# Kernel optimization log

Hardware: AMD Instinct MI355X
Metric: run time of the kernel (lower is better)

The kernel has to match this reference:

```python
import jax, jax.numpy as jnp
import numpy as np

N = 50000       # nodes
E = 800000      # edges (before self-loops)
NFEAT = 256
NHID = 16       # per-head hidden dim
HEADS = 8
NCLASS = 16
NEG_SLOPE = 0.2  # PyG GATConv default leaky-relu slope


def setup_inputs() -> dict:
    key = jax.random.key(0)
    ks = jax.random.split(key, 10)
    s = 0.05  # weight scale for numerical sanity
    return {
        "x": jax.random.normal(ks[0], (N, NFEAT), jnp.float32),
        "edge_index": jax.random.randint(ks[1], (2, E), 0, N, dtype=jnp.int32),
        "W1": jax.random.normal(ks[2], (NFEAT, HEADS * NHID), jnp.float32) * s,
        "att_src1": jax.random.normal(ks[3], (HEADS, NHID), jnp.float32) * s,
        "att_dst1": jax.random.normal(ks[4], (HEADS, NHID), jnp.float32) * s,
        "b1": jnp.zeros((HEADS * NHID,), jnp.float32),
        "W2": jax.random.normal(ks[5], (HEADS * NHID, NCLASS), jnp.float32) * s,
        "att_src2": jax.random.normal(ks[6], (1, NCLASS), jnp.float32) * s,
        "att_dst2": jax.random.normal(ks[7], (1, NCLASS), jnp.float32) * s,
        "b2": jnp.zeros((NCLASS,), jnp.float32),
    }


def gat_conv(x, edge_index, W, a_src, a_dst, b, heads, out_c, concat):
    """Faithful PyG GATConv (eval mode: dropout off, add_self_loops=True)."""
    n = x.shape[0]
    loop = jnp.arange(n, dtype=edge_index.dtype)
    src = jnp.concatenate([edge_index[0], loop])  # [E+N]
    dst = jnp.concatenate([edge_index[1], loop])  # [E+N]
    h = (x @ W).reshape(n, heads, out_c)          # [N, H, C]
    # per-node attention logits
    alpha_src = jnp.einsum('nhc,hc->nh', h, a_src)  # [N, H]
    alpha_dst = jnp.einsum('nhc,hc->nh', h, a_dst)  # [N, H]
    e = jax.nn.leaky_relu(alpha_src[src] + alpha_dst[dst], NEG_SLOPE)  # [E+N, H]
    # segment softmax over incoming edges of each dst node (self-loop guarantees nonempty)
    m = jax.lax.stop_gradient(jax.ops.segment_max(e, dst, num_segments=n))
    p = jnp.exp(e - m[dst])
    denom = jax.ops.segment_sum(p, dst, num_segments=n)
    a = p / denom[dst]                              # [E+N, H]
    out = jax.ops.segment_sum(a[:, :, None] * h[src], dst, num_segments=n)  # [N, H, C]
    out = out.reshape(n, heads * out_c) if concat else out.mean(axis=1)
    return out + b


def reference(x, edge_index, W1, att_src1, att_dst1, b1, W2, att_src2, att_dst2, b2):
    h1 = jax.nn.elu(gat_conv(x, edge_index, W1, att_src1, att_dst1, b1, HEADS, NHID, True))
    return gat_conv(h1, edge_index, W2, att_src2, att_dst2, b2, 1, NCLASS, False)
```

## Files before the change

kernel.cpp:

```cpp
#include <hip/hip_runtime.h>
#include <hip/hip_bf16.h>

#define NNODES 50000
#define NEDGES 800000
#define NFEATS 256
#define NHID 16
#define HEADS 8
#define NCLS 16
#define NEG_SLOPE 0.2f
#define TOTE (NEDGES + NNODES)
#define RSTRIDE 64
#define NBUCK 196
#define NPB 256
#define BCAP 4864
#define S1_EPT 16

typedef __attribute__((ext_vector_type(8))) short short8;
typedef __attribute__((ext_vector_type(4))) float floatx4;

static __device__ __forceinline__ short f2bf(float f) {
    __hip_bfloat16 b = __float2bfloat16(f);
    return *reinterpret_cast<short*>(&b);
}

#define AS1 __attribute__((address_space(1)))
#define AS3 __attribute__((address_space(3)))

static __device__ __forceinline__ void ld_lds16(const void* g, void* l) {
#if __has_builtin(__builtin_amdgcn_global_load_lds)
    __builtin_amdgcn_global_load_lds((const AS1 void*)g, (AS3 void*)l, 16, 0, 0);
#endif
}


__global__ __launch_bounds__(256) void k_bin(const int* __restrict__ ei,
                                             int* __restrict__ gcnt, int2* __restrict__ barr) {
    __shared__ int lcnt[NBUCK], lbase[NBUCK];
    int tid = threadIdx.x;
    if (tid < NBUCK) lcnt[tid] = 0;
    __syncthreads();
    int e0 = blockIdx.x * (256 * S1_EPT) + tid;
    int s[S1_EPT], d[S1_EPT], rk[S1_EPT];
#pragma unroll
    for (int k = 0; k < S1_EPT; k++) {
        int e = e0 + k * 256;
        bool v = e < TOTE;
        int ss = 0, dd = 0;
        if (v) {
            if (e < NEDGES) { ss = ei[e]; dd = ei[NEDGES + e]; }
            else            { ss = e - NEDGES; dd = ss; }
        }
        s[k] = ss; d[k] = dd;
        rk[k] = v ? atomicAdd(&lcnt[dd >> 8], 1) : -1;
    }
    __syncthreads();
    if (tid < NBUCK) lbase[tid] = lcnt[tid] ? atomicAdd(&gcnt[tid], lcnt[tid]) : 0;
    __syncthreads();
#pragma unroll
    for (int k = 0; k < S1_EPT; k++) {
        if (rk[k] >= 0) {
            int b = d[k] >> 8;
            int pos = lbase[b] + rk[k];
            if (pos < BCAP) barr[(size_t)b * BCAP + pos] = make_int2(s[k], d[k]);
        }
    }
}


__global__ __launch_bounds__(256) void k_csr(const int* __restrict__ gcnt,
                                             const int2* __restrict__ barr,
                                             int* __restrict__ cnt, int* __restrict__ csr) {
    __shared__ int lcnt[NPB];
    __shared__ unsigned short lcsr[NPB * 65];
    int b = blockIdx.x, tid = threadIdx.x;
    lcnt[tid] = 0;
    __syncthreads();
    int n = min(gcnt[b], BCAP);
    int nodeBase = b << 8;
    for (int i = tid; i < n; i += 256) {
        int2 e = barr[(size_t)b * BCAP + i];
        int ln = e.y - nodeBase;
        int r = atomicAdd(&lcnt[ln], 1);
        if (r < RSTRIDE) lcsr[ln * 65 + r] = (unsigned short)e.x;
    }
    __syncthreads();
    int node = nodeBase + tid;
    if (node < NNODES) cnt[node] = min(lcnt[tid], RSTRIDE);
    for (int i = tid; i < NPB * RSTRIDE; i += 256) {
        int nn = nodeBase + (i >> 6);
        if (nn < NNODES)
            csr[(size_t)nodeBase * RSTRIDE + i] = (int)lcsr[(i >> 6) * 65 + (i & 63)];
    }
}


__global__ void k_prepw(const float* __restrict__ W, const float* __restrict__ a_s,
                        const float* __restrict__ a_d, short* __restrict__ Wsw) {
    int t = blockIdx.x * 256 + threadIdx.x;
    if (t >= 4608) return;
    short8 b;
    if (t < 4096) {
        int kc = t >> 9, nt = (t >> 6) & 7, lane = t & 63;
        int quad = lane >> 4, lo = lane & 15;
#pragma unroll
        for (int j = 0; j < 8; j++)
            b[j] = f2bf(W[(size_t)(kc * 32 + quad * 8 + j) * 128 + nt * 16 + lo]);
    } else {
        int t2 = t - 4096;
        int kc = t2 >> 6, lane = t2 & 63;
        int quad = lane >> 4, lo = lane & 15;
        int h = lo & 7;
        const float* av = (lo < 8) ? (a_s + h * 16) : (a_d + h * 16);
#pragma unroll
        for (int j = 0; j < 8; j++) {
            int k = kc * 32 + quad * 8 + j;
            float acc = 0.f;
#pragma unroll
            for (int c = 0; c < 16; c++) acc += W[(size_t)k * 128 + h * 16 + c] * av[c];
            b[j] = f2bf(acc);
        }
    }
    *(short8*)(Wsw + (size_t)t * 8) = b;
}


__global__ __launch_bounds__(256) void k_gemm1(const float* __restrict__ x,
                                               const short* __restrict__ Wsw,
                                               __hip_bfloat16* __restrict__ h1,
                                               float* __restrict__ as1, float* __restrict__ ad1) {
    __shared__ short bsw[32768];
    int tid  = threadIdx.x;
    int wave = tid >> 6;
    int lane = tid & 63;
    int quad = lane >> 4;
    int lo   = lane & 15;

#if __has_builtin(__builtin_amdgcn_global_load_lds)
    {
        const char* gsrc = (const char*)Wsw + (size_t)wave * 1024 + (size_t)lane * 16;
        char* ldst = (char*)bsw + wave * 1024;
#pragma unroll
        for (int it = 0; it < 16; it++)
            ld_lds16(gsrc + it * 4096, ldst + it * 4096);
    }
#else
    {
        const uint4* g4 = (const uint4*)Wsw;
        uint4* l4 = (uint4*)bsw;
#pragma unroll
        for (int it = 0; it < 16; it++) l4[it * 256 + tid] = g4[it * 256 + tid];
    }
#endif
    short8 wafr[8];
#pragma unroll
    for (int kc = 0; kc < 8; kc++)
        wafr[kc] = *(const short8*)(Wsw + (size_t)(4096 + kc * 64 + lane) * 8);
    __syncthreads();

    int rowBase = blockIdx.x * 128 + wave * 32;
    const float* xa[2];
#pragma unroll
    for (int mt = 0; mt < 2; mt++) {
        int row = rowBase + mt * 16 + lo;
        row = (row < NNODES) ? row : (NNODES - 1);
        xa[mt] = x + (size_t)row * 256 + quad * 8;
    }

    floatx4 acc[2][8], accA[2];
#pragma unroll
    for (int mt = 0; mt < 2; mt++) {
        accA[mt] = (floatx4){0.f, 0.f, 0.f, 0.f};
#pragma unroll
        for (int nt = 0; nt < 8; nt++) acc[mt][nt] = (floatx4){0.f, 0.f, 0.f, 0.f};
    }

    float4 a0[2], a1[2];
#pragma unroll
    for (int mt = 0; mt < 2; mt++) {
        a0[mt] = *(const float4*)(xa[mt]);
        a1[mt] = *(const float4*)(xa[mt] + 4);
    }

    for (int kc = 0; kc < 8; kc++) {
        float4 n0[2], n1[2];
        if (kc < 7) {
#pragma unroll
            for (int mt = 0; mt < 2; mt++) {
                n0[mt] = *(const float4*)(xa[mt] + (kc + 1) * 32);
                n1[mt] = *(const float4*)(xa[mt] + (kc + 1) * 32 + 4);
            }
        }
        short8 afr[2];
#pragma unroll
        for (int mt = 0; mt < 2; mt++) {
            union { short8 s; __hip_bfloat162 h[4]; } u;
            u.h[0] = __float22bfloat162_rn(make_float2(a0[mt].x, a0[mt].y));
            u.h[1] = __float22bfloat162_rn(make_float2(a0[mt].z, a0[mt].w));
            u.h[2] = __float22bfloat162_rn(make_float2(a1[mt].x, a1[mt].y));
            u.h[3] = __float22bfloat162_rn(make_float2(a1[mt].z, a1[mt].w));
            afr[mt] = u.s;
        }
#pragma unroll
        for (int nt = 0; nt < 8; nt++) {
            short8 bfr = *(const short8*)&bsw[((kc * 8 + nt) * 64 + lane) * 8];
            acc[0][nt] = __builtin_amdgcn_mfma_f32_16x16x32_bf16(afr[0], bfr, acc[0][nt], 0, 0, 0);
            acc[1][nt] = __builtin_amdgcn_mfma_f32_16x16x32_bf16(afr[1], bfr, acc[1][nt], 0, 0, 0);
        }
        accA[0] = __builtin_amdgcn_mfma_f32_16x16x32_bf16(afr[0], wafr[kc], accA[0], 0, 0, 0);
        accA[1] = __builtin_amdgcn_mfma_f32_16x16x32_bf16(afr[1], wafr[kc], accA[1], 0, 0, 0);
#pragma unroll
        for (int mt = 0; mt < 2; mt++) { a0[mt] = n0[mt]; a1[mt] = n1[mt]; }
    }

#pragma unroll
    for (int mt = 0; mt < 2; mt++)
#pragma unroll
        for (int nt = 0; nt < 8; nt++)
#pragma unroll
            for (int reg = 0; reg < 4; reg++) {
                int row = rowBase + mt * 16 + quad * 4 + reg;
                int col = nt * 16 + lo;
                if (row < NNODES)
                    h1[(size_t)row * 128 + col] = __float2bfloat16(acc[mt][nt][reg]);
            }
#pragma unroll
    for (int mt = 0; mt < 2; mt++)
#pragma unroll
        for (int reg = 0; reg < 4; reg++) {
            int row = rowBase + mt * 16 + quad * 4 + reg;
            if (row < NNODES) {
                float v = accA[mt][reg];
                if (lo < 8) as1[(size_t)row * 8 + lo] = v;
                else        ad1[(size_t)row * 8 + (lo - 8)] = v;
            }
        }
}


__global__ __launch_bounds__(256) void k_agg1(const int* __restrict__ cnt, const int* __restrict__ csr,
                                              const __hip_bfloat16* __restrict__ h1,
                                              const float* __restrict__ as1, const float* __restrict__ ad1,
                                              const float* __restrict__ b1, __hip_bfloat16* __restrict__ h1act) {
    int node = blockIdx.x * 4 + (threadIdx.x >> 6);
    int lane = threadIdx.x & 63;
    if (node >= NNODES) return;
    int rs = node * RSTRIDE;
    int deg = min(cnt[node], RSTRIDE);
    int slot = lane >> 4;
    int cl   = lane & 15;
    int head = cl >> 1;
    float adst = ad1[node * 8 + head];

    float acc[8] = {0.f, 0.f, 0.f, 0.f, 0.f, 0.f, 0.f, 0.f};
    float s = 0.f;
    for (int base = 0; base < deg; base += 8) {
        int i0 = base + slot, i1 = base + 4 + slot;
        float p0 = 0.f, p1 = 0.f;
        union { short8 v; __hip_bfloat162 h[4]; } u0, u1;
        u0.v = (short8){0, 0, 0, 0, 0, 0, 0, 0};
        u1.v = (short8){0, 0, 0, 0, 0, 0, 0, 0};
        if (i0 < deg) {
            int sa = csr[rs + i0];
            u0.v = *(const short8*)(h1 + (size_t)sa * 128 + cl * 8);
            float e0 = as1[sa * 8 + head] + adst;
            e0 = (e0 > 0.f) ? e0 : NEG_SLOPE * e0;
            p0 = __expf(e0);
        }
        if (i1 < deg) {
            int sb = csr[rs + i1];
            u1.v = *(const short8*)(h1 + (size_t)sb * 128 + cl * 8);
            float e1 = as1[sb * 8 + head] + adst;
            e1 = (e1 > 0.f) ? e1 : NEG_SLOPE * e1;
            p1 = __expf(e1);
        }
        s += p0 + p1;
#pragma unroll
        for (int q = 0; q < 4; q++) {
            float2 f0 = __bfloat1622float2(u0.h[q]);
            float2 f1 = __bfloat1622float2(u1.h[q]);
            acc[q * 2]     = fmaf(p0, f0.x, fmaf(p1, f1.x, acc[q * 2]));
            acc[q * 2 + 1] = fmaf(p0, f0.y, fmaf(p1, f1.y, acc[q * 2 + 1]));
        }
    }
#pragma unroll
    for (int q = 0; q < 8; q++) {
        acc[q] += __shfl_xor(acc[q], 16);
        acc[q] += __shfl_xor(acc[q], 32);
    }
    s += __shfl_xor(s, 16);
    s += __shfl_xor(s, 32);
    if (slot == 0) {
        float is = 1.f / s;
        union { short8 v; short us[8]; } pk;
#pragma unroll
        for (int q = 0; q < 8; q++) {
            float v = acc[q] * is + b1[cl * 8 + q];
            v = (v > 0.f) ? v : (__expf(v) - 1.f);
            pk.us[q] = f2bf(v);
        }
        *(short8*)(h1act + (size_t)node * 128 + cl * 8) = pk.v;
    }
}


__global__ __launch_bounds__(256) void k_gemm2(const __hip_bfloat16* __restrict__ h1act,
                                               const float* __restrict__ W2,
                                               const float* __restrict__ a_src,
                                               const float* __restrict__ a_dst,
                                               float* __restrict__ h2,
                                               float* __restrict__ as2, float* __restrict__ ad2) {
    __shared__ float w[128 * 16];
    __shared__ float hr[16][129];
    int tid = threadIdx.x;
    int row0 = blockIdx.x * 16;
    for (int i = tid; i < 2048; i += 256) w[i] = W2[i];
    {
        int r = tid >> 4, k8 = (tid & 15) * 8;
        int gr = row0 + r;
        union { short8 v; __hip_bfloat162 h[4]; } u;
        if (gr < NNODES) u.v = *(const short8*)(h1act + (size_t)gr * 128 + k8);
        else             u.v = (short8){0, 0, 0, 0, 0, 0, 0, 0};
#pragma unroll
        for (int q = 0; q < 4; q++) {
            float2 f = __bfloat1622float2(u.h[q]);
            hr[r][k8 + q * 2]     = f.x;
            hr[r][k8 + q * 2 + 1] = f.y;
        }
    }
    __syncthreads();
    int r = tid >> 4, c = tid & 15;
    float acc = 0.f;
#pragma unroll 8
    for (int k = 0; k < 128; k++) acc += hr[r][k] * w[k * 16 + c];
    int gr = row0 + r;
    if (gr < NNODES) h2[(size_t)gr * 16 + c] = acc;
    float sv = acc * a_src[c];
    float dv = acc * a_dst[c];
#pragma unroll
    for (int o = 1; o <= 8; o <<= 1) {
        sv += __shfl_xor(sv, o);
        dv += __shfl_xor(dv, o);
    }
    if (c == 0 && gr < NNODES) { as2[gr] = sv; ad2[gr] = dv; }
}


__global__ __launch_bounds__(256) void k_agg2(const int* __restrict__ cnt, const int* __restrict__ csr,
                                              const float* __restrict__ h2, const float* __restrict__ as2,
                                              const float* __restrict__ ad2, const float* __restrict__ b2,
                                              float* __restrict__ out) {
    int node = blockIdx.x * 4 + (threadIdx.x >> 6);
    int lane = threadIdx.x & 63;
    if (node >= NNODES) return;
    int rs = node * RSTRIDE;
    int deg = min(cnt[node], RSTRIDE);
    int slot = lane >> 2;
    int c4   = lane & 3;
    float adst = ad2[node];

    float4 acc = make_float4(0.f, 0.f, 0.f, 0.f);
    float s = 0.f;
    for (int base = 0; base < deg; base += 16) {
        int i0 = base + slot;
        float p0 = 0.f;
        float4 r0 = make_float4(0.f, 0.f, 0.f, 0.f);
        if (i0 < deg) {
            int sa = csr[rs + i0];
            r0 = *(const float4*)(h2 + (size_t)sa * 16 + c4 * 4);
            float e0 = as2[sa] + adst;
            e0 = (e0 > 0.f) ? e0 : NEG_SLOPE * e0;
            p0 = __expf(e0);
        }
        s += p0;
        acc.x = fmaf(p0, r0.x, acc.x);
        acc.y = fmaf(p0, r0.y, acc.y);
        acc.z = fmaf(p0, r0.z, acc.z);
        acc.w = fmaf(p0, r0.w, acc.w);
    }
#pragma unroll
    for (int o = 4; o <= 32; o <<= 1) {
        acc.x += __shfl_xor(acc.x, o);
        acc.y += __shfl_xor(acc.y, o);
        acc.z += __shfl_xor(acc.z, o);
        acc.w += __shfl_xor(acc.w, o);
        s += __shfl_xor(s, o);
    }
    if (slot == 0) {
        float is = 1.f / s;
        float4 o4;
        o4.x = acc.x * is + b2[c4 * 4 + 0];
        o4.y = acc.y * is + b2[c4 * 4 + 1];
        o4.z = acc.z * is + b2[c4 * 4 + 2];
        o4.w = acc.w * is + b2[c4 * 4 + 3];
        *(float4*)(out + (size_t)node * 16 + c4 * 4) = o4;
    }
}


extern "C" void kernel_launch(void* const* d_in, const int* in_sizes, int n_in,
                              void* d_out, int out_size, void* d_ws, size_t ws_size,
                              hipStream_t stream) {
    const float* x    = (const float*)d_in[0];
    const int*   ei   = (const int*)d_in[1];
    const float* W1   = (const float*)d_in[2];
    const float* a_s1 = (const float*)d_in[3];
    const float* a_d1 = (const float*)d_in[4];
    const float* b1   = (const float*)d_in[5];
    const float* W2   = (const float*)d_in[6];
    const float* a_s2 = (const float*)d_in[7];
    const float* a_d2 = (const float*)d_in[8];
    const float* b2   = (const float*)d_in[9];
    float* out = (float*)d_out;

    char* p = (char*)d_ws;
    auto alloc = [&](size_t bytes) -> char* {
        char* q = p;
        p += (bytes + 255) & ~(size_t)255;
        return q;
    };
    int*  gcnt = (int*)alloc(NBUCK * 4);
    int2* barr = (int2*)alloc((size_t)NBUCK * BCAP * 8);
    int*  cnt  = (int*)alloc((size_t)NNODES * 4);
    int*  csr  = (int*)alloc((size_t)NNODES * RSTRIDE * 4);
    short* Wsw = (short*)alloc((size_t)36864 * 2);
    __hip_bfloat16* h1 = (__hip_bfloat16*)alloc((size_t)NNODES * 128 * 2);
    float* as1 = (float*)alloc((size_t)NNODES * 8 * 4);
    float* ad1 = (float*)alloc((size_t)NNODES * 8 * 4);
    __hip_bfloat16* h1act = (__hip_bfloat16*)alloc((size_t)NNODES * 128 * 2);
    float* h2  = (float*)as1;
    float* as2 = (float*)barr;
    float* ad2 = (float*)(barr + NNODES);

    hipMemsetAsync(gcnt, 0, NBUCK * 4, stream);
    hipLaunchKernelGGL(k_bin,   dim3((TOTE + 4095) / 4096), dim3(256), 0, stream, ei, gcnt, barr);
    hipLaunchKernelGGL(k_csr,   dim3(NBUCK), dim3(256), 0, stream, gcnt, barr, cnt, csr);
    hipLaunchKernelGGL(k_prepw, dim3(18), dim3(256), 0, stream, W1, a_s1, a_d1, Wsw);
    hipLaunchKernelGGL(k_gemm1, dim3((NNODES + 127) / 128), dim3(256), 0, stream, x, Wsw, h1, as1, ad1);
    hipLaunchKernelGGL(k_agg1,  dim3((NNODES + 3) / 4), dim3(256), 0, stream, cnt, csr, h1, as1, ad1, b1, h1act);
    hipLaunchKernelGGL(k_gemm2, dim3((NNODES + 15) / 16), dim3(256), 0, stream, h1act, W2, a_s2, a_d2, h2, as2, ad2);
    hipLaunchKernelGGL(k_agg2,  dim3((NNODES + 3) / 4), dim3(256), 0, stream, cnt, csr, h2, as2, ad2, b2, out);
}
```

Measured before the change: 229.2 us.

## Pack binned edges into 32-bit words and preload CSR rows via wave shuffles

Edge bins now store a single 32-bit word (local dst in the high half, src in the low 16 bits) instead of an int2, halving bucket traffic. CSR writes skip slots beyond each node's degree. Both aggregation kernels load the whole 64-entry CSR row once per lane and broadcast neighbour indices with shuffles. They also process more edges per iteration (4 per slot in agg1, 2 in agg2) to expose more memory parallelism. Packing the source into 16 bits only works if node ids fit in 16 bits. With 50000 nodes they do, since the previous code already truncated sources to unsigned short, and the later reuse of barr for as2/ad2 still fits.

```diff
diff --git a/kernel.cpp b/kernel.cpp
--- a/kernel.cpp
+++ b/kernel.cpp
@@ -34,7 +34,7 @@
 
 
 __global__ __launch_bounds__(256) void k_bin(const int* __restrict__ ei,
-                                             int* __restrict__ gcnt, int2* __restrict__ barr) {
+                                             int* __restrict__ gcnt, int* __restrict__ barr) {
     __shared__ int lcnt[NBUCK], lbase[NBUCK];
     int tid = threadIdx.x;
     if (tid < NBUCK) lcnt[tid] = 0;
@@ -61,14 +61,15 @@
         if (rk[k] >= 0) {
             int b = d[k] >> 8;
             int pos = lbase[b] + rk[k];
-            if (pos < BCAP) barr[(size_t)b * BCAP + pos] = make_int2(s[k], d[k]);
+            if (pos < BCAP)
+                barr[(size_t)b * BCAP + pos] = ((d[k] & 255) << 16) | s[k];
         }
     }
 }
 
 
 __global__ __launch_bounds__(256) void k_csr(const int* __restrict__ gcnt,
-                                             const int2* __restrict__ barr,
+                                             const int* __restrict__ barr,
                                              int* __restrict__ cnt, int* __restrict__ csr) {
     __shared__ int lcnt[NPB];
     __shared__ unsigned short lcsr[NPB * 65];
@@ -78,18 +79,19 @@
     int n = min(gcnt[b], BCAP);
     int nodeBase = b << 8;
     for (int i = tid; i < n; i += 256) {
-        int2 e = barr[(size_t)b * BCAP + i];
-        int ln = e.y - nodeBase;
+        int e = barr[(size_t)b * BCAP + i];
+        int ln = e >> 16;
         int r = atomicAdd(&lcnt[ln], 1);
-        if (r < RSTRIDE) lcsr[ln * 65 + r] = (unsigned short)e.x;
+        if (r < RSTRIDE) lcsr[ln * 65 + r] = (unsigned short)(e & 0xFFFF);
     }
     __syncthreads();
     int node = nodeBase + tid;
     if (node < NNODES) cnt[node] = min(lcnt[tid], RSTRIDE);
     for (int i = tid; i < NPB * RSTRIDE; i += 256) {
-        int nn = nodeBase + (i >> 6);
-        if (nn < NNODES)
-            csr[(size_t)nodeBase * RSTRIDE + i] = (int)lcsr[(i >> 6) * 65 + (i & 63)];
+        int ln = i >> 6;
+        int nn = nodeBase + ln;
+        if (nn < NNODES && (i & 63) < min(lcnt[ln], RSTRIDE))
+            csr[(size_t)nodeBase * RSTRIDE + i] = (int)lcsr[ln * 65 + (i & 63)];
     }
 }
 
@@ -250,37 +252,36 @@
     int cl   = lane & 15;
     int head = cl >> 1;
     float adst = ad1[node * 8 + head];
+    int rowv = csr[rs + lane];
 
     float acc[8] = {0.f, 0.f, 0.f, 0.f, 0.f, 0.f, 0.f, 0.f};
     float s = 0.f;
-    for (int base = 0; base < deg; base += 8) {
-        int i0 = base + slot, i1 = base + 4 + slot;
-        float p0 = 0.f, p1 = 0.f;
-        union { short8 v; __hip_bfloat162 h[4]; } u0, u1;
-        u0.v = (short8){0, 0, 0, 0, 0, 0, 0, 0};
-        u1.v = (short8){0, 0, 0, 0, 0, 0, 0, 0};
-        if (i0 < deg) {
-            int sa = csr[rs + i0];
-            u0.v = *(const short8*)(h1 + (size_t)sa * 128 + cl * 8);
-            float e0 = as1[sa * 8 + head] + adst;
-            e0 = (e0 > 0.f) ? e0 : NEG_SLOPE * e0;
-            p0 = __expf(e0);
-        }
-        if (i1 < deg) {
-            int sb = csr[rs + i1];
-            u1.v = *(const short8*)(h1 + (size_t)sb * 128 + cl * 8);
-            float e1 = as1[sb * 8 + head] + adst;
-            e1 = (e1 > 0.f) ? e1 : NEG_SLOPE * e1;
-            p1 = __expf(e1);
-        }
-        s += p0 + p1;
-#pragma unroll
-        for (int q = 0; q < 4; q++) {
-            float2 f0 = __bfloat1622float2(u0.h[q]);
-            float2 f1 = __bfloat1622float2(u1.h[q]);
-            acc[q * 2]     = fmaf(p0, f0.x, fmaf(p1, f1.x, acc[q * 2]));
-            acc[q * 2 + 1] = fmaf(p0, f0.y, fmaf(p1, f1.y, acc[q * 2 + 1]));
-        }
+    for (int base = 0; base < deg; base += 16) {
+        int src[4]; float p[4];
+        union { short8 v; __hip_bfloat162 h[4]; } u[4];
+#pragma unroll
+        for (int t = 0; t < 4; t++)
+            src[t] = __shfl(rowv, base + slot + t * 4);
+#pragma unroll
+        for (int t = 0; t < 4; t++) {
+            p[t] = 0.f;
+            u[t].v = (short8){0, 0, 0, 0, 0, 0, 0, 0};
+            if (base + slot + t * 4 < deg) {
+                u[t].v = *(const short8*)(h1 + (size_t)src[t] * 128 + cl * 8);
+                float e = as1[src[t] * 8 + head] + adst;
+                e = (e > 0.f) ? e : NEG_SLOPE * e;
+                p[t] = __expf(e);
+            }
+        }
+        s += (p[0] + p[1]) + (p[2] + p[3]);
+#pragma unroll
+        for (int t = 0; t < 4; t++)
+#pragma unroll
+            for (int q = 0; q < 4; q++) {
+                float2 f = __bfloat1622float2(u[t].h[q]);
+                acc[q * 2]     = fmaf(p[t], f.x, acc[q * 2]);
+                acc[q * 2 + 1] = fmaf(p[t], f.y, acc[q * 2 + 1]);
+            }
     }
 #pragma unroll
     for (int q = 0; q < 8; q++) {
@@ -357,25 +358,34 @@
     int slot = lane >> 2;
     int c4   = lane & 3;
     float adst = ad2[node];
+    int rowv = csr[rs + lane];
 
     float4 acc = make_float4(0.f, 0.f, 0.f, 0.f);
     float s = 0.f;
-    for (int base = 0; base < deg; base += 16) {
-        int i0 = base + slot;
-        float p0 = 0.f;
+    for (int base = 0; base < deg; base += 32) {
+        int i0 = base + slot, i1 = base + 16 + slot;
+        int sa = __shfl(rowv, i0);
+        int sb = __shfl(rowv, i1);
+        float p0 = 0.f, p1 = 0.f;
         float4 r0 = make_float4(0.f, 0.f, 0.f, 0.f);
+        float4 r1 = make_float4(0.f, 0.f, 0.f, 0.f);
         if (i0 < deg) {
-            int sa = csr[rs + i0];
             r0 = *(const float4*)(h2 + (size_t)sa * 16 + c4 * 4);
-            float e0 = as2[sa] + adst;
-            e0 = (e0 > 0.f) ? e0 : NEG_SLOPE * e0;
-            p0 = __expf(e0);
-        }
-        s += p0;
-        acc.x = fmaf(p0, r0.x, acc.x);
-        acc.y = fmaf(p0, r0.y, acc.y);
-        acc.z = fmaf(p0, r0.z, acc.z);
-        acc.w = fmaf(p0, r0.w, acc.w);
+            float e = as2[sa] + adst;
+            e = (e > 0.f) ? e : NEG_SLOPE * e;
+            p0 = __expf(e);
+        }
+        if (i1 < deg) {
+            r1 = *(const float4*)(h2 + (size_t)sb * 16 + c4 * 4);
+            float e = as2[sb] + adst;
+            e = (e > 0.f) ? e : NEG_SLOPE * e;
+            p1 = __expf(e);
+        }
+        s += p0 + p1;
+        acc.x = fmaf(p0, r0.x, fmaf(p1, r1.x, acc.x));
+        acc.y = fmaf(p0, r0.y, fmaf(p1, r1.y, acc.y));
+        acc.z = fmaf(p0, r0.z, fmaf(p1, r1.z, acc.z));
+        acc.w = fmaf(p0, r0.w, fmaf(p1, r1.w, acc.w));
     }
 #pragma unroll
     for (int o = 4; o <= 32; o <<= 1) {
@@ -419,7 +429,7 @@
         return q;
     };
     int*  gcnt = (int*)alloc(NBUCK * 4);
-    int2* barr = (int2*)alloc((size_t)NBUCK * BCAP * 8);
+    int*  barr = (int*)alloc((size_t)NBUCK * BCAP * 4);
     int*  cnt  = (int*)alloc((size_t)NNODES * 4);
     int*  csr  = (int*)alloc((size_t)NNODES * RSTRIDE * 4);
     short* Wsw = (short*)alloc((size_t)36864 * 2);
@@ -429,7 +439,7 @@
     __hip_bfloat16* h1act = (__hip_bfloat16*)alloc((size_t)NNODES * 128 * 2);
     float* h2  = (float*)as1;
     float* as2 = (float*)barr;
-    float* ad2 = (float*)(barr + NNODES);
+    float* ad2 = (float*)barr + NNODES;
 
     hipMemsetAsync(gcnt, 0, NBUCK * 4, stream);
     hipLaunchKernelGGL(k_bin,   dim3((TOTE + 4095) / 4096), dim3(256), 0, stream, ei, gcnt, barr);
```

Result: no change. 225.8 us (-1.5%).
